# Kernel tuning notes

Measured on AMD Instinct MI355X. Metric: run time of the kernel, lower is better.

## Reference

```python
import jax, jax.numpy as jnp
import numpy as np


def reference(x, phi, sigma, M_phi_plus, M_phi_minus, M_u, padded_sl):
    """STU forward: spectral FFT convolution + autoregressive input term.

    x:   (B, L, D) input sequence
    phi: (L, K) time-domain spectral filters (top-K Hankel eigenvectors);
         V = rfft(phi, n=padded_sl) matches the module's precomputed V.
    sigma: (K,) Hankel eigenvalues
    M_phi_plus/minus: (K, D, D) per-filter projections
    M_u: (k_u, D, D) AR-on-input matrices
    """
    B, L, D = x.shape
    K = sigma.shape[0]
    n = padded_sl  # FFT length for causal linear convolution

    # Alternating-sign trick for the 'minus' featurization:
    # sum_j (-1)^j phi_j u_{t-j} = (-1)^t * conv(phi, sgn*u)_t
    sgn = jnp.where(jnp.arange(L) % 2 == 0, 1.0, -1.0).astype(x.dtype)[None, :, None]  # (1,L,1)

    V = jnp.fft.rfft(phi, n=n, axis=0)                       # (n//2+1, K) complex
    U = jnp.fft.rfft(jnp.stack([x, x * sgn], axis=-1), n=n, axis=1)  # (B, n//2+1, D, 2)
    prod = V[None, :, :, None, None] * U[:, :, None, :, :]    # (B, n//2+1, K, D, 2)
    conv = jnp.fft.irfft(prod, n=n, axis=1)[:, :L]            # (B, L, K, D, 2) causal conv
    U_plus = conv[..., 0]
    U_minus = conv[..., 1] * sgn[..., None]                   # undo sign on output side

    # Fold sigma^{1/4} scaling into the projection matrices.
    sig4 = (sigma ** 0.25).astype(x.dtype)[:, None, None]     # (K,1,1)
    spectral = (
        jnp.einsum('blkd,kdo->blo', U_plus, M_phi_plus * sig4)
        + jnp.einsum('blkd,kdo->blo', U_minus, M_phi_minus * sig4)
    )

    # compute_ar_u: y_t += sum_{i=0}^{k_u-1} x_{t-i} @ M_u[i]  (use_ar_u=True)
    ar_u = jnp.einsum('bld,do->blo', x, M_u[0])
    for i in range(1, M_u.shape[0]):  # small fixed depth k_u=3
        x_shift = jnp.pad(x, ((0, 0), (i, 0), (0, 0)))[:, :L]
        ar_u = ar_u + jnp.einsum('bld,do->blo', x_shift, M_u[i])

    # use_ar_y=False branch; dropout=0 (identity)
    return spectral + ar_u


def setup_inputs() -> dict:
    key = jax.random.key(0)
    ks = jax.random.split(key, 6)
    B, L, D, K, KU, N = 1, 2048, 768, 16, 3, 4096
    x = jax.random.normal(ks[0], (B, L, D), jnp.float32)
    phi = jax.random.normal(ks[1], (L, K), jnp.float32) / np.sqrt(L).astype(np.float32)
    sigma = jax.random.uniform(ks[2], (K,), jnp.float32, 0.1, 1.0)
    M_phi_plus = jax.random.normal(ks[3], (K, D, D), jnp.float32) * 0.02
    M_phi_minus = jax.random.normal(ks[4], (K, D, D), jnp.float32) * 0.02
    M_u = jax.random.normal(ks[5], (KU, D, D), jnp.float32) * 0.02
    return {"x": x, "phi": phi, "sigma": sigma, "M_phi_plus": M_phi_plus,
            "M_phi_minus": M_phi_minus, "M_u": M_u, "padded_sl": N}
```

## Files before the change

### kernel.cpp

```cpp
#include <hip/hip_runtime.h>

typedef __attribute__((ext_vector_type(8))) short bf16x8;
typedef __attribute__((ext_vector_type(8))) short short8;
typedef __attribute__((ext_vector_type(4))) float f32x4;

#define SL 2048
#define DM 768
#define NCH 32
#define MSPEC 24576
#define MTOT  26880

#define SPLITK 10
#define KSLICE 2688
#define NT2 42
#define NITER2 21

#define WS_U      0
#define WS_TMAT   110100480ULL
#define WS_XT     126910464ULL
#define WS_MCAT   130056192ULL
#define WS_PART   171343872ULL
#define WS_NEED   234258432ULL

#define NB_M   5040
#define NB_T   4104
#define NB_AR  768
#define NB_XT  384
#define NB_ALL (NB_M + NB_T + NB_AR + NB_XT)

__device__ __forceinline__ short f2bf(float f) {
  unsigned u = __builtin_bit_cast(unsigned, f);
  u = (u + 0x7FFFu + ((u >> 16) & 1u)) >> 16;
  return (short)u;
}

__device__ __forceinline__ void gload16(const short* g, short* l) {
  __builtin_amdgcn_global_load_lds(
      (const __attribute__((address_space(1))) void*)g,
      (__attribute__((address_space(3))) void*)l, 16, 0, 0);
}


__global__ __launch_bounds__(256) void k_zero(float4* out) {
  out[blockIdx.x * 256 + threadIdx.x] = float4{0.f, 0.f, 0.f, 0.f};
}

__global__ __launch_bounds__(256) void k_prep_all(const float* __restrict__ x,
                                                  const float* __restrict__ phi,
                                                  const float* __restrict__ sigma,
                                                  const float* __restrict__ Mp,
                                                  const float* __restrict__ Mm,
                                                  const float* __restrict__ Mu,
                                                  short* __restrict__ xT,
                                                  short* __restrict__ U,
                                                  short* __restrict__ Tmat,
                                                  short* __restrict__ McatT) {
  __shared__ short tile[64][65];
  const int b = blockIdx.x;
  const int t = threadIdx.x;

  if (b < NB_M) {
    const int m0 = (b % 420) * 64, o0 = (b / 420) * 64;
#pragma unroll
    for (int rr = 0; rr < 16; ++rr) {
      int ml = rr * 4 + (t >> 6), ol = t & 63;
      int m = m0 + ml, o = o0 + ol;
      float v;
      if (m < MSPEC) {
        int c = m / DM, d = m - c * DM;
        int k = c & 15;
        float s4 = sqrtf(sqrtf(sigma[k]));
        if (c < 16) v = Mp[((size_t)c * DM + d) * DM + o] * s4;
        else        v = Mm[((size_t)(c - 16) * DM + d) * DM + o] * s4;
      } else {
        int mm = m - MSPEC;
        int i = mm / DM, d = mm - i * DM;
        v = Mu[((size_t)i * DM + d) * DM + o];
      }
      tile[ml][ol] = f2bf(v);
    }
    __syncthreads();
#pragma unroll
    for (int rr = 0; rr < 16; ++rr) {
      int ol = rr * 4 + (t >> 6), ml = t & 63;
      McatT[(size_t)(o0 + ol) * MTOT + m0 + ml] = tile[ml][ol];
    }
    return;
  }
  if (b < NB_M + NB_T) {
    int idx = ((b - NB_M) * 256 + t) * 8;
    int c = idx >> 18;
    short8 v = {0, 0, 0, 0, 0, 0, 0, 0};
    if (c < 32) {
      int b0 = idx & 127, a = (idx >> 7) & 127, dlag = (idx >> 14) & 15;
      int j0 = dlag * 128 + a - b0;
#pragma unroll
      for (int e = 0; e < 8; ++e) {
        int j = j0 - e;
        if (j >= 0) {
          float p = phi[j * 16 + (c & 15)];
          if (c >= 16 && (j & 1)) p = -p;
          v[e] = f2bf(p);
        }
      }
    }
    *reinterpret_cast<short8*>(&Tmat[idx]) = v;
    return;
  }
  if (b < NB_M + NB_T + NB_AR) {
    int tid = (b - NB_M - NB_T) * 256 + t;
    int l = tid / 96, d0 = (tid - l * 96) * 8;
#pragma unroll
    for (int i = 0; i < 3; ++i) {
      short8 v = {0, 0, 0, 0, 0, 0, 0, 0};
      if (l >= i) {
        const float* src = &x[(size_t)(l - i) * DM + d0];
#pragma unroll
        for (int e = 0; e < 8; ++e) v[e] = f2bf(src[e]);
      }
      *reinterpret_cast<short8*>(&U[(size_t)l * MTOT + MSPEC + i * DM + d0]) = v;
    }
    return;
  }
  {
    const int bb = b - NB_M - NB_T - NB_AR;
    const int d0 = (bb % 12) * 64, l0 = (bb / 12) * 64;
#pragma unroll
    for (int rr = 0; rr < 16; ++rr) {
      int ll = rr * 4 + (t >> 6), dl = t & 63;
      tile[ll][dl] = f2bf(x[(size_t)(l0 + ll) * DM + d0 + dl]);
    }
    __syncthreads();
#pragma unroll
    for (int rr = 0; rr < 16; ++rr) {
      int dl = rr * 4 + (t >> 6), ll = t & 63;
      xT[(size_t)(d0 + dl) * SL + l0 + ll] = tile[ll][dl];
    }
  }
}


#define LDSREADS(BUF, KS, MQ)                                                   \
    _Pragma("unroll")                                                           \
    for (int q_ = 0; q_ < 4; ++q_)                                              \
      af_[q_] = *reinterpret_cast<const bf16x8*>(                               \
          &As[BUF][KS][wm1][((MQ) * 64 + q_ * 16 + lrow) * 32 + foff]);         \
    if ((MQ) == 0) {                                                            \
      _Pragma("unroll")                                                         \
      for (int i_ = 0; i_ < 4; ++i_)                                            \
        bf_[i_] = *reinterpret_cast<const bf16x8*>(                             \
            &Bs[BUF][KS][hB][(rB0 + i_ * 16 + lrow) * 32 + foff]);              \
    }

#define DOMFMA(MQ)                                                              \
    _Pragma("unroll")                                                           \
    for (int q_ = 0; q_ < 4; ++q_)                                              \
      _Pragma("unroll")                                                         \
      for (int i_ = 0; i_ < 4; ++i_)                                            \
        acc[(MQ) * 4 + q_][i_] = __builtin_amdgcn_mfma_f32_16x16x32_bf16(       \
            af_[q_], bf_[i_], acc[(MQ) * 4 + q_][i_], 0, 0, 0)

#define PHASE(BUF, KS, MQ, VMODE, STG) do {                                     \
    bf16x8 af_[4];                                                              \
    if ((VMODE) == 1) asm volatile("s_waitcnt vmcnt(6)" ::: "memory");          \
    if ((VMODE) == 2) {                                                         \
      if (j < nIterM1) asm volatile("s_waitcnt vmcnt(6)" ::: "memory");         \
      else             asm volatile("s_waitcnt vmcnt(0)" ::: "memory");         \
    }                                                                           \
    if ((VMODE) == 0) { LDSREADS(BUF, KS, MQ) }                                 \
    STG;                                                                        \
    if ((VMODE) != 0) {                                                         \
      __builtin_amdgcn_s_barrier();                                             \
      asm volatile("" ::: "memory");                                            \
      LDSREADS(BUF, KS, MQ)                                                     \
    }                                                                           \
    __builtin_amdgcn_s_setprio(1);                                              \
    DOMFMA(MQ);                                                                 \
    __builtin_amdgcn_s_setprio(0);                                              \
    asm volatile("s_waitcnt lgkmcnt(0)" ::: "memory");                          \
    __builtin_amdgcn_s_barrier();                                               \
  } while (0)


#define STA1(SBUF, SKS, SKT) do { int kt_ = (SKT); if (kt_ < nT) {              \
    int kch_ = kt_ * 64 + (SKS) * 32;                                           \
    int kb_ = kch_ >> 7, bo_ = kch_ & 127;                                      \
    int dl_ = 2 * rt - kb_;                                                     \
    const short* g0_ = (dl_ >= 0) ? (Tc + ((size_t)dl_ << 14) + bo_)            \
                                  : (Tz + bo_);                                 \
    const short* g1_ = Tc + ((size_t)(dl_ + 1) << 14) + bo_;                    \
    gload16(g0_, &As[SBUF][SKS][0][t8]);                                        \
    gload16(g1_, &As[SBUF][SKS][1][t8]); } } while (0)

#define STB1(SBUF, SKS, SKT) do { int kt_ = (SKT); if (kt_ < nT) {              \
    const short* g_ = Bb + kt_ * 64 + (SKS) * 32;                               \
    gload16(g_, &Bs[SBUF][SKS][0][t8]);                                         \
    gload16(g_ + (size_t)128 * SL, &Bs[SBUF][SKS][1][t8]); } } while (0)

__global__ __launch_bounds__(512, 2) void k_gemm1_8p(const short* __restrict__ Tmat,
                                                     const short* __restrict__ xT,
                                                     short* __restrict__ U) {
  __shared__ __align__(16) short As[2][2][2][4096];
  __shared__ __align__(16) short Bs[2][2][2][4096];
  const int bid = blockIdx.x;
  const int xcd = bid & 7;
  const int slot = bid >> 3;
  const int c = xcd * 4 + (slot & 3);
  const int q = slot >> 2;
  const int ct = q % 3;
  const int rt = 7 - q / 3;
  const int nT = 4 * (rt + 1);
  const int nIter = 2 * (rt + 1);
  const int nIterM1 = nIter - 1;
  const int t = threadIdx.x;
  const int lane = t & 63, wave = t >> 6;
  const int wm1 = wave >> 2;
  const int hB = (wave & 3) >> 1;
  const int rB0 = (wave & 1) * 64;
  const int lrow = lane & 15, quad = lane >> 4;
  const int foff = (quad ^ ((lrow >> 1) & 3)) << 3;
  const int r = t >> 2;
  const int cswz = ((t & 3) ^ ((r >> 1) & 3)) << 3;
  const int t8 = t * 8;

  const short* Tc = Tmat + ((size_t)(c * 16) << 14) + r * 128 + cswz;
  const short* Tz = Tmat + ((size_t)512 << 14) + r * 128 + cswz;
  const short* Bb = xT + (size_t)(ct * 256 + r) * SL + cswz;

  f32x4 acc[8][4] = {};

  STB1(0, 0, 0); STA1(0, 0, 0); STB1(0, 1, 0); STA1(0, 1, 0);
  STB1(1, 0, 1); STA1(1, 0, 1); STB1(1, 1, 1);

  for (int j = 0; j < nIter; ++j) {
    bf16x8 bf_[4];
    PHASE(0, 0, 0, 1, STA1(1, 1, 2 * j + 1));
    PHASE(0, 0, 1, 0, STB1(0, 0, 2 * j + 2));
    PHASE(0, 1, 0, 0, STA1(0, 0, 2 * j + 2));
    PHASE(0, 1, 1, 0, STB1(0, 1, 2 * j + 2));
    PHASE(1, 0, 0, 2, STA1(0, 1, 2 * j + 2));
    PHASE(1, 0, 1, 0, STB1(1, 0, 2 * j + 3));
    PHASE(1, 1, 0, 0, STA1(1, 0, 2 * j + 3));
    PHASE(1, 1, 1, 0, STB1(1, 1, 2 * j + 3));
  }

  const int wm128 = (wave >> 2) * 128, wn64 = (wave & 3) * 64;
  const int l0 = rt * 256, colbase = c * DM + ct * 256;
#pragma unroll
  for (int im = 0; im < 8; ++im)
#pragma unroll
    for (int in = 0; in < 4; ++in)
#pragma unroll
      for (int r4 = 0; r4 < 4; ++r4) {
        int row = l0 + wm128 + im * 16 + quad * 4 + r4;
        int col = colbase + wn64 + in * 16 + lrow;
        U[(size_t)row * MTOT + col] = f2bf(acc[im][in][r4]);
      }
}


#define STA2(SBUF, SKS, SKT) do { int kt_ = (SKT); if (kt_ < NT2) {             \
    const short* g_ = Abase + kt_ * 64 + (SKS) * 32;                            \
    gload16(g_, &As[SBUF][SKS][0][t8]);                                         \
    gload16(g_ + (size_t)128 * MTOT, &As[SBUF][SKS][1][t8]); } } while (0)

#define STB2(SBUF, SKS, SKT) do { int kt_ = (SKT); if (kt_ < NT2) {             \
    const short* g_ = Bbase + kt_ * 64 + (SKS) * 32;                            \
    gload16(g_, &Bs[SBUF][SKS][0][t8]);                                         \
    gload16(g_ + (size_t)128 * MTOT, &Bs[SBUF][SKS][1][t8]); } } while (0)

__global__ __launch_bounds__(512, 2) void k_gemm2_8p(const short* __restrict__ U,
                                                     const short* __restrict__ McatT,
                                                     float* __restrict__ out,
                                                     float* __restrict__ part,
                                                     int use_part) {
  __shared__ __align__(16) short As[2][2][2][4096];
  __shared__ __align__(16) short Bs[2][2][2][4096];
  const int bid = blockIdx.x;
  const int tile = bid % 24, kc = bid / 24;
  const int mt = tile & 7, nt_ = tile >> 3;
  const int m0 = mt * 256, o0 = nt_ * 256;
  const int kbase = kc * KSLICE;
  const int t = threadIdx.x;
  const int lane = t & 63, wave = t >> 6;
  const int wm1 = wave >> 2;
  const int hB = (wave & 3) >> 1;
  const int rB0 = (wave & 1) * 64;
  const int lrow = lane & 15, quad = lane >> 4;
  const int foff = (quad ^ ((lrow >> 1) & 3)) << 3;
  const int r = t >> 2;
  const int cswz = ((t & 3) ^ ((r >> 1) & 3)) << 3;
  const int t8 = t * 8;
  const int nIterM1 = NITER2 - 1;

  const short* Abase = U     + (size_t)(m0 + r) * MTOT + kbase + cswz;
  const short* Bbase = McatT + (size_t)(o0 + r) * MTOT + kbase + cswz;

  f32x4 acc[8][4] = {};

  STB2(0, 0, 0); STA2(0, 0, 0); STB2(0, 1, 0); STA2(0, 1, 0);
  STB2(1, 0, 1); STA2(1, 0, 1); STB2(1, 1, 1);

  for (int j = 0; j < NITER2; ++j) {
    bf16x8 bf_[4];
    PHASE(0, 0, 0, 1, STA2(1, 1, 2 * j + 1));
    PHASE(0, 0, 1, 0, STB2(0, 0, 2 * j + 2));
    PHASE(0, 1, 0, 0, STA2(0, 0, 2 * j + 2));
    PHASE(0, 1, 1, 0, STB2(0, 1, 2 * j + 2));
    PHASE(1, 0, 0, 2, STA2(0, 1, 2 * j + 2));
    PHASE(1, 0, 1, 0, STB2(1, 0, 2 * j + 3));
    PHASE(1, 1, 0, 0, STA2(1, 0, 2 * j + 3));
    PHASE(1, 1, 1, 0, STB2(1, 1, 2 * j + 3));
  }

  const int wm128 = (wave >> 2) * 128, wn64 = (wave & 3) * 64;
  if (use_part) {
    float* dst = part + (size_t)kc * (2048 * 768);
#pragma unroll
    for (int im = 0; im < 8; ++im)
#pragma unroll
      for (int in = 0; in < 4; ++in)
#pragma unroll
        for (int r4 = 0; r4 < 4; ++r4) {
          int row = m0 + wm128 + im * 16 + quad * 4 + r4;
          int col = o0 + wn64 + in * 16 + lrow;
          dst[(size_t)row * DM + col] = acc[im][in][r4];
        }
  } else {
#pragma unroll
    for (int im = 0; im < 8; ++im)
#pragma unroll
      for (int in = 0; in < 4; ++in)
#pragma unroll
        for (int r4 = 0; r4 < 4; ++r4) {
          int row = m0 + wm128 + im * 16 + quad * 4 + r4;
          int col = o0 + wn64 + in * 16 + lrow;
          atomicAdd(&out[(size_t)row * DM + col], acc[im][in][r4]);
        }
  }
}

__global__ __launch_bounds__(256) void k_reduce(const float4* __restrict__ part,
                                                float4* __restrict__ out) {
  int i = blockIdx.x * 256 + threadIdx.x;
  float4 s = part[i];
#pragma unroll
  for (int k = 1; k < SPLITK; ++k) {
    float4 v = part[(size_t)k * 393216 + i];
    s.x += v.x; s.y += v.y; s.z += v.z; s.w += v.w;
  }
  out[i] = s;
}

extern "C" void kernel_launch(void* const* d_in, const int* in_sizes, int n_in,
                              void* d_out, int out_size, void* d_ws, size_t ws_size,
                              hipStream_t stream) {
  (void)in_sizes; (void)n_in; (void)out_size;
  const float* x     = (const float*)d_in[0];
  const float* phi   = (const float*)d_in[1];
  const float* sigma = (const float*)d_in[2];
  const float* Mp    = (const float*)d_in[3];
  const float* Mm    = (const float*)d_in[4];
  const float* Mu    = (const float*)d_in[5];
  float* out = (float*)d_out;
  char* ws = (char*)d_ws;

  short* U     = (short*)(ws + WS_U);
  short* Tmat  = (short*)(ws + WS_TMAT);
  short* xT    = (short*)(ws + WS_XT);
  short* McatT = (short*)(ws + WS_MCAT);
  float* Wpart = (float*)(ws + WS_PART);
  const int use_part = ws_size >= WS_NEED ? 1 : 0;

  if (!use_part)
    k_zero<<<dim3(1536), dim3(256), 0, stream>>>((float4*)out);
  k_prep_all<<<dim3(NB_ALL), dim3(256), 0, stream>>>(x, phi, sigma, Mp, Mm, Mu,
                                                     xT, U, Tmat, McatT);
  k_gemm1_8p<<<dim3(768), dim3(512), 0, stream>>>(Tmat, xT, U);
  k_gemm2_8p<<<dim3(240), dim3(512), 0, stream>>>(U, McatT, out, Wpart, use_part);
  if (use_part)
    k_reduce<<<dim3(1536), dim3(256), 0, stream>>>((const float4*)Wpart, (float4*)out);
}
```

Baseline: 367.3 us.

## Transpose MFMA operands for vectorized epilogue stores and branchless clamped tile loads

Swaps the A/B operands of the MFMA so each lane holds four consecutive output columns. The GEMM epilogues can then write packed short4 bf16 and float4 partials instead of scalar strided stores. The Toeplitz matrix layout gains a leading zero block per channel (17 blocks instead of 16), so negative-lag loads read real zeros without a separate pointer. Out-of-range tile loads are clamped to the last tile instead of branched around, which removes divergent conditionals at the cost of redundant loads and a slightly larger workspace.

```diff
diff --git a/kernel.cpp b/kernel.cpp
--- a/kernel.cpp
+++ b/kernel.cpp
@@ -2,6 +2,7 @@
 
 typedef __attribute__((ext_vector_type(8))) short bf16x8;
 typedef __attribute__((ext_vector_type(8))) short short8;
+typedef __attribute__((ext_vector_type(4))) short short4v;
 typedef __attribute__((ext_vector_type(4))) float f32x4;
 
 #define SL 2048
@@ -15,15 +16,15 @@
 #define NT2 42
 #define NITER2 21
 
-#define WS_U      0
+#define WS_U      0ULL
 #define WS_TMAT   110100480ULL
-#define WS_XT     126910464ULL
-#define WS_MCAT   130056192ULL
-#define WS_PART   171343872ULL
-#define WS_NEED   234258432ULL
+#define WS_XT     127926272ULL
+#define WS_MCAT   131072000ULL
+#define WS_PART   172359680ULL
+#define WS_NEED   235274240ULL
 
 #define NB_M   5040
-#define NB_T   4104
+#define NB_T   4352
 #define NB_AR  768
 #define NB_XT  384
 #define NB_ALL (NB_M + NB_T + NB_AR + NB_XT)
@@ -89,10 +90,13 @@
   }
   if (b < NB_M + NB_T) {
     int idx = ((b - NB_M) * 256 + t) * 8;
-    int c = idx >> 18;
+    int blk = idx >> 14;
+    int c = blk / 17;
+    int w = blk - c * 17;
     short8 v = {0, 0, 0, 0, 0, 0, 0, 0};
-    if (c < 32) {
-      int b0 = idx & 127, a = (idx >> 7) & 127, dlag = (idx >> 14) & 15;
+    if (w > 0) {
+      int dlag = w - 1;
+      int b0 = idx & 127, a = (idx >> 7) & 127;
       int j0 = dlag * 128 + a - b0;
 #pragma unroll
       for (int e = 0; e < 8; ++e) {
@@ -158,7 +162,7 @@
       _Pragma("unroll")                                                         \
       for (int i_ = 0; i_ < 4; ++i_)                                            \
         acc[(MQ) * 4 + q_][i_] = __builtin_amdgcn_mfma_f32_16x16x32_bf16(       \
-            af_[q_], bf_[i_], acc[(MQ) * 4 + q_][i_], 0, 0, 0)
+            bf_[i_], af_[q_], acc[(MQ) * 4 + q_][i_], 0, 0, 0)
 
 #define PHASE(BUF, KS, MQ, VMODE, STG) do {                                     \
     bf16x8 af_[4];                                                              \
@@ -182,20 +186,19 @@
   } while (0)
 
 
-#define STA1(SBUF, SKS, SKT) do { int kt_ = (SKT); if (kt_ < nT) {              \
+#define STA1(SBUF, SKS, SKT) do {                                               \
+    int kt_ = (SKT); kt_ = kt_ < nTm1 ? kt_ : nTm1;                             \
     int kch_ = kt_ * 64 + (SKS) * 32;                                           \
     int kb_ = kch_ >> 7, bo_ = kch_ & 127;                                      \
-    int dl_ = 2 * rt - kb_;                                                     \
-    const short* g0_ = (dl_ >= 0) ? (Tc + ((size_t)dl_ << 14) + bo_)            \
-                                  : (Tz + bo_);                                 \
-    const short* g1_ = Tc + ((size_t)(dl_ + 1) << 14) + bo_;                    \
+    const short* g0_ = Tc + ((size_t)(2 * rt - kb_) << 14) + bo_;               \
     gload16(g0_, &As[SBUF][SKS][0][t8]);                                        \
-    gload16(g1_, &As[SBUF][SKS][1][t8]); } } while (0)
-
-#define STB1(SBUF, SKS, SKT) do { int kt_ = (SKT); if (kt_ < nT) {              \
+    gload16(g0_ + 16384, &As[SBUF][SKS][1][t8]); } while (0)
+
+#define STB1(SBUF, SKS, SKT) do {                                               \
+    int kt_ = (SKT); kt_ = kt_ < nTm1 ? kt_ : nTm1;                             \
     const short* g_ = Bb + kt_ * 64 + (SKS) * 32;                               \
     gload16(g_, &Bs[SBUF][SKS][0][t8]);                                         \
-    gload16(g_ + (size_t)128 * SL, &Bs[SBUF][SKS][1][t8]); } } while (0)
+    gload16(g_ + (size_t)128 * SL, &Bs[SBUF][SKS][1][t8]); } while (0)
 
 __global__ __launch_bounds__(512, 2) void k_gemm1_8p(const short* __restrict__ Tmat,
                                                      const short* __restrict__ xT,
@@ -210,6 +213,7 @@
   const int ct = q % 3;
   const int rt = 7 - q / 3;
   const int nT = 4 * (rt + 1);
+  const int nTm1 = nT - 1;
   const int nIter = 2 * (rt + 1);
   const int nIterM1 = nIter - 1;
   const int t = threadIdx.x;
@@ -223,8 +227,7 @@
   const int cswz = ((t & 3) ^ ((r >> 1) & 3)) << 3;
   const int t8 = t * 8;
 
-  const short* Tc = Tmat + ((size_t)(c * 16) << 14) + r * 128 + cswz;
-  const short* Tz = Tmat + ((size_t)512 << 14) + r * 128 + cswz;
+  const short* Tc = Tmat + ((size_t)(c * 17 + 1) << 14) + r * 128 + cswz;
   const short* Bb = xT + (size_t)(ct * 256 + r) * SL + cswz;
 
   f32x4 acc[8][4] = {};
@@ -247,27 +250,31 @@
   const int wm128 = (wave >> 2) * 128, wn64 = (wave & 3) * 64;
   const int l0 = rt * 256, colbase = c * DM + ct * 256;
 #pragma unroll
-  for (int im = 0; im < 8; ++im)
-#pragma unroll
-    for (int in = 0; in < 4; ++in)
-#pragma unroll
-      for (int r4 = 0; r4 < 4; ++r4) {
-        int row = l0 + wm128 + im * 16 + quad * 4 + r4;
-        int col = colbase + wn64 + in * 16 + lrow;
-        U[(size_t)row * MTOT + col] = f2bf(acc[im][in][r4]);
-      }
-}
-
-
-#define STA2(SBUF, SKS, SKT) do { int kt_ = (SKT); if (kt_ < NT2) {             \
+  for (int im = 0; im < 8; ++im) {
+    int row = l0 + wm128 + im * 16 + lrow;
+#pragma unroll
+    for (int in = 0; in < 4; ++in) {
+      int col = colbase + wn64 + in * 16 + quad * 4;
+      short4v v;
+#pragma unroll
+      for (int r4 = 0; r4 < 4; ++r4) v[r4] = f2bf(acc[im][in][r4]);
+      *reinterpret_cast<short4v*>(&U[(size_t)row * MTOT + col]) = v;
+    }
+  }
+}
+
+
+#define STA2(SBUF, SKS, SKT) do {                                               \
+    int kt_ = (SKT); kt_ = kt_ < NT2 - 1 ? kt_ : NT2 - 1;                       \
     const short* g_ = Abase + kt_ * 64 + (SKS) * 32;                            \
     gload16(g_, &As[SBUF][SKS][0][t8]);                                         \
-    gload16(g_ + (size_t)128 * MTOT, &As[SBUF][SKS][1][t8]); } } while (0)
-
-#define STB2(SBUF, SKS, SKT) do { int kt_ = (SKT); if (kt_ < NT2) {             \
+    gload16(g_ + (size_t)128 * MTOT, &As[SBUF][SKS][1][t8]); } while (0)
+
+#define STB2(SBUF, SKS, SKT) do {                                               \
+    int kt_ = (SKT); kt_ = kt_ < NT2 - 1 ? kt_ : NT2 - 1;                       \
     const short* g_ = Bbase + kt_ * 64 + (SKS) * 32;                            \
     gload16(g_, &Bs[SBUF][SKS][0][t8]);                                         \
-    gload16(g_ + (size_t)128 * MTOT, &Bs[SBUF][SKS][1][t8]); } } while (0)
+    gload16(g_ + (size_t)128 * MTOT, &Bs[SBUF][SKS][1][t8]); } while (0)
 
 __global__ __launch_bounds__(512, 2) void k_gemm2_8p(const short* __restrict__ U,
                                                      const short* __restrict__ McatT,
@@ -317,26 +324,27 @@
   if (use_part) {
     float* dst = part + (size_t)kc * (2048 * 768);
 #pragma unroll
-    for (int im = 0; im < 8; ++im)
-#pragma unroll
-      for (int in = 0; in < 4; ++in)
-#pragma unroll
-        for (int r4 = 0; r4 < 4; ++r4) {
-          int row = m0 + wm128 + im * 16 + quad * 4 + r4;
-          int col = o0 + wn64 + in * 16 + lrow;
-          dst[(size_t)row * DM + col] = acc[im][in][r4];
-        }
+    for (int im = 0; im < 8; ++im) {
+      int row = m0 + wm128 + im * 16 + lrow;
+#pragma unroll
+      for (int in = 0; in < 4; ++in) {
+        int col = o0 + wn64 + in * 16 + quad * 4;
+        float4 v = {acc[im][in][0], acc[im][in][1], acc[im][in][2], acc[im][in][3]};
+        *reinterpret_cast<float4*>(&dst[(size_t)row * DM + col]) = v;
+      }
+    }
   } else {
 #pragma unroll
-    for (int im = 0; im < 8; ++im)
-#pragma unroll
-      for (int in = 0; in < 4; ++in)
-#pragma unroll
-        for (int r4 = 0; r4 < 4; ++r4) {
-          int row = m0 + wm128 + im * 16 + quad * 4 + r4;
-          int col = o0 + wn64 + in * 16 + lrow;
-          atomicAdd(&out[(size_t)row * DM + col], acc[im][in][r4]);
-        }
+    for (int im = 0; im < 8; ++im) {
+      int row = m0 + wm128 + im * 16 + lrow;
+#pragma unroll
+      for (int in = 0; in < 4; ++in) {
+        int col = o0 + wn64 + in * 16 + quad * 4;
+#pragma unroll
+        for (int r4 = 0; r4 < 4; ++r4)
+          atomicAdd(&out[(size_t)row * DM + col + r4], acc[im][in][r4]);
+      }
+    }
   }
 }
 
```

Result: slower. 383.2 us (+4.3%).

## Replace 8-phase gemm2 pipeline with simple double-buffered loop and split-K 21

Applied to the files above, without the earlier changes.

The second GEMM drops its 8-phase, 4-stage software pipeline in favour of a plain double-buffered loop over 32-wide K steps, with a __syncthreads per step. Shared memory per block is halved and launch bounds now allow 4 blocks per CU. When the workspace is large enough, split-K goes from 10 to 21 (504 blocks) to fill the GPU better, at the cost of more partial-sum traffic in the reduce. The simpler pipeline gives up much of the latency hiding within a block and depends on higher occupancy to cover it instead.

```diff
diff --git a/kernel.cpp b/kernel.cpp
--- a/kernel.cpp
+++ b/kernel.cpp
@@ -10,17 +10,13 @@
 #define MSPEC 24576
 #define MTOT  26880
 
-#define SPLITK 10
-#define KSLICE 2688
-#define NT2 42
-#define NITER2 21
-
-#define WS_U      0
+#define WS_U      0ULL
 #define WS_TMAT   110100480ULL
 #define WS_XT     126910464ULL
 #define WS_MCAT   130056192ULL
 #define WS_PART   171343872ULL
-#define WS_NEED   234258432ULL
+#define WS_NEED10 234258432ULL
+#define WS_NEED21 303464448ULL
 
 #define NB_M   5040
 #define NB_T   4104
@@ -259,28 +255,18 @@
 }
 
 
-#define STA2(SBUF, SKS, SKT) do { int kt_ = (SKT); if (kt_ < NT2) {             \
-    const short* g_ = Abase + kt_ * 64 + (SKS) * 32;                            \
-    gload16(g_, &As[SBUF][SKS][0][t8]);                                         \
-    gload16(g_ + (size_t)128 * MTOT, &As[SBUF][SKS][1][t8]); } } while (0)
-
-#define STB2(SBUF, SKS, SKT) do { int kt_ = (SKT); if (kt_ < NT2) {             \
-    const short* g_ = Bbase + kt_ * 64 + (SKS) * 32;                            \
-    gload16(g_, &Bs[SBUF][SKS][0][t8]);                                         \
-    gload16(g_ + (size_t)128 * MTOT, &Bs[SBUF][SKS][1][t8]); } } while (0)
-
-__global__ __launch_bounds__(512, 2) void k_gemm2_8p(const short* __restrict__ U,
+template<int KSL, int NS>
+__global__ __launch_bounds__(512, 4) void k_gemm2_2p(const short* __restrict__ U,
                                                      const short* __restrict__ McatT,
                                                      float* __restrict__ out,
                                                      float* __restrict__ part,
                                                      int use_part) {
-  __shared__ __align__(16) short As[2][2][2][4096];
-  __shared__ __align__(16) short Bs[2][2][2][4096];
+  __shared__ __align__(16) short As[2][2][4096];
+  __shared__ __align__(16) short Bs[2][2][4096];
   const int bid = blockIdx.x;
   const int tile = bid % 24, kc = bid / 24;
   const int mt = tile & 7, nt_ = tile >> 3;
   const int m0 = mt * 256, o0 = nt_ * 256;
-  const int kbase = kc * KSLICE;
   const int t = threadIdx.x;
   const int lane = t & 63, wave = t >> 6;
   const int wm1 = wave >> 2;
@@ -291,31 +277,57 @@
   const int r = t >> 2;
   const int cswz = ((t & 3) ^ ((r >> 1) & 3)) << 3;
   const int t8 = t * 8;
-  const int nIterM1 = NITER2 - 1;
-
-  const short* Abase = U     + (size_t)(m0 + r) * MTOT + kbase + cswz;
-  const short* Bbase = McatT + (size_t)(o0 + r) * MTOT + kbase + cswz;
+
+  const short* Abase = U     + (size_t)(m0 + r) * MTOT + kc * KSL + cswz;
+  const short* Bbase = McatT + (size_t)(o0 + r) * MTOT + kc * KSL + cswz;
 
   f32x4 acc[8][4] = {};
 
-  STB2(0, 0, 0); STA2(0, 0, 0); STB2(0, 1, 0); STA2(0, 1, 0);
-  STB2(1, 0, 1); STA2(1, 0, 1); STB2(1, 1, 1);
-
-  for (int j = 0; j < NITER2; ++j) {
-    bf16x8 bf_[4];
-    PHASE(0, 0, 0, 1, STA2(1, 1, 2 * j + 1));
-    PHASE(0, 0, 1, 0, STB2(0, 0, 2 * j + 2));
-    PHASE(0, 1, 0, 0, STA2(0, 0, 2 * j + 2));
-    PHASE(0, 1, 1, 0, STB2(0, 1, 2 * j + 2));
-    PHASE(1, 0, 0, 2, STA2(0, 1, 2 * j + 2));
-    PHASE(1, 0, 1, 0, STB2(1, 0, 2 * j + 3));
-    PHASE(1, 1, 0, 0, STA2(1, 0, 2 * j + 3));
-    PHASE(1, 1, 1, 0, STB2(1, 1, 2 * j + 3));
+  auto stA = [&](int buf, int s) {
+    const short* g = Abase + s * 32;
+    gload16(g, &As[buf][0][t8]);
+    gload16(g + (size_t)128 * MTOT, &As[buf][1][t8]);
+  };
+  auto stB = [&](int buf, int s) {
+    const short* g = Bbase + s * 32;
+    gload16(g, &Bs[buf][0][t8]);
+    gload16(g + (size_t)128 * MTOT, &Bs[buf][1][t8]);
+  };
+
+  stA(0, 0); stB(0, 0);
+  int cur = 0;
+  for (int s = 0; s < NS; ++s) {
+    __syncthreads();
+    if (s + 1 < NS) { stA(cur ^ 1, s + 1); stB(cur ^ 1, s + 1); }
+    bf16x8 af0[4], af1[4], bf[4];
+#pragma unroll
+    for (int i = 0; i < 4; ++i)
+      bf[i] = *reinterpret_cast<const bf16x8*>(
+          &Bs[cur][hB][(rB0 + i * 16 + lrow) * 32 + foff]);
+#pragma unroll
+    for (int q = 0; q < 4; ++q)
+      af0[q] = *reinterpret_cast<const bf16x8*>(
+          &As[cur][wm1][(q * 16 + lrow) * 32 + foff]);
+#pragma unroll
+    for (int q = 0; q < 4; ++q)
+      af1[q] = *reinterpret_cast<const bf16x8*>(
+          &As[cur][wm1][(64 + q * 16 + lrow) * 32 + foff]);
+#pragma unroll
+    for (int q = 0; q < 4; ++q)
+#pragma unroll
+      for (int i = 0; i < 4; ++i)
+        acc[q][i] = __builtin_amdgcn_mfma_f32_16x16x32_bf16(af0[q], bf[i], acc[q][i], 0, 0, 0);
+#pragma unroll
+    for (int q = 0; q < 4; ++q)
+#pragma unroll
+      for (int i = 0; i < 4; ++i)
+        acc[4 + q][i] = __builtin_amdgcn_mfma_f32_16x16x32_bf16(af1[q], bf[i], acc[4 + q][i], 0, 0, 0);
+    cur ^= 1;
   }
 
   const int wm128 = (wave >> 2) * 128, wn64 = (wave & 3) * 64;
   if (use_part) {
-    float* dst = part + (size_t)kc * (2048 * 768);
+    float* dst = part + (size_t)kc * (SL * DM);
 #pragma unroll
     for (int im = 0; im < 8; ++im)
 #pragma unroll
@@ -341,11 +353,10 @@
 }
 
 __global__ __launch_bounds__(256) void k_reduce(const float4* __restrict__ part,
-                                                float4* __restrict__ out) {
+                                                float4* __restrict__ out, int nk) {
   int i = blockIdx.x * 256 + threadIdx.x;
   float4 s = part[i];
-#pragma unroll
-  for (int k = 1; k < SPLITK; ++k) {
+  for (int k = 1; k < nk; ++k) {
     float4 v = part[(size_t)k * 393216 + i];
     s.x += v.x; s.y += v.y; s.z += v.z; s.w += v.w;
   }
@@ -370,14 +381,21 @@
   short* xT    = (short*)(ws + WS_XT);
   short* McatT = (short*)(ws + WS_MCAT);
   float* Wpart = (float*)(ws + WS_PART);
-  const int use_part = ws_size >= WS_NEED ? 1 : 0;
-
-  if (!use_part)
+
+  const int mode = (ws_size >= WS_NEED21) ? 21 : (ws_size >= WS_NEED10 ? 10 : 0);
+
+  if (mode == 0)
     k_zero<<<dim3(1536), dim3(256), 0, stream>>>((float4*)out);
   k_prep_all<<<dim3(NB_ALL), dim3(256), 0, stream>>>(x, phi, sigma, Mp, Mm, Mu,
                                                      xT, U, Tmat, McatT);
   k_gemm1_8p<<<dim3(768), dim3(512), 0, stream>>>(Tmat, xT, U);
-  k_gemm2_8p<<<dim3(240), dim3(512), 0, stream>>>(U, McatT, out, Wpart, use_part);
-  if (use_part)
-    k_reduce<<<dim3(1536), dim3(256), 0, stream>>>((const float4*)Wpart, (float4*)out);
-}
+  if (mode == 21) {
+    k_gemm2_2p<1280, 40><<<dim3(504), dim3(512), 0, stream>>>(U, McatT, out, Wpart, 1);
+    k_reduce<<<dim3(1536), dim3(256), 0, stream>>>((const float4*)Wpart, (float4*)out, 21);
+  } else if (mode == 10) {
+    k_gemm2_2p<2688, 84><<<dim3(240), dim3(512), 0, stream>>>(U, McatT, out, Wpart, 1);
+    k_reduce<<<dim3(1536), dim3(256), 0, stream>>>((const float4*)Wpart, (float4*)out, 10);
+  } else {
+    k_gemm2_2p<2688, 84><<<dim3(240), dim3(512), 0, stream>>>(U, McatT, out, Wpart, 0);
+  }
+}
```

Result: slower. 753.2 us (+105.1%).

## Replace second GEMM with smaller-tile 128x128 split-K-8 kernel using simple double buffering

Applied to the files above, without the earlier changes.

Swaps the heavily pipelined 256x256-tile, split-K-10 second GEMM (240 blocks of 512 threads) for a 128x128-tile, split-K-8 kernel with 768 blocks of 256 threads. Each block double-buffers 32-wide K steps, with one barrier per step. The aim is more blocks to fill the CUs and fewer partial buffers to reduce. In exchange, each tile reuses data less, the loads and MFMAs overlap less finely, and more barriers are hit per unit of work.

```diff
diff --git a/kernel.cpp b/kernel.cpp
--- a/kernel.cpp
+++ b/kernel.cpp
@@ -10,12 +10,7 @@
 #define MSPEC 24576
 #define MTOT  26880
 
-#define SPLITK 10
-#define KSLICE 2688
-#define NT2 42
-#define NITER2 21
-
-#define WS_U      0
+#define WS_U      0ULL
 #define WS_TMAT   110100480ULL
 #define WS_XT     126910464ULL
 #define WS_MCAT   130056192ULL
@@ -259,93 +254,91 @@
 }
 
 
-#define STA2(SBUF, SKS, SKT) do { int kt_ = (SKT); if (kt_ < NT2) {             \
-    const short* g_ = Abase + kt_ * 64 + (SKS) * 32;                            \
-    gload16(g_, &As[SBUF][SKS][0][t8]);                                         \
-    gload16(g_ + (size_t)128 * MTOT, &As[SBUF][SKS][1][t8]); } } while (0)
-
-#define STB2(SBUF, SKS, SKT) do { int kt_ = (SKT); if (kt_ < NT2) {             \
-    const short* g_ = Bbase + kt_ * 64 + (SKS) * 32;                            \
-    gload16(g_, &Bs[SBUF][SKS][0][t8]);                                         \
-    gload16(g_ + (size_t)128 * MTOT, &Bs[SBUF][SKS][1][t8]); } } while (0)
-
-__global__ __launch_bounds__(512, 2) void k_gemm2_8p(const short* __restrict__ U,
-                                                     const short* __restrict__ McatT,
-                                                     float* __restrict__ out,
-                                                     float* __restrict__ part,
-                                                     int use_part) {
-  __shared__ __align__(16) short As[2][2][2][4096];
-  __shared__ __align__(16) short Bs[2][2][2][4096];
-  const int bid = blockIdx.x;
-  const int tile = bid % 24, kc = bid / 24;
-  const int mt = tile & 7, nt_ = tile >> 3;
-  const int m0 = mt * 256, o0 = nt_ * 256;
-  const int kbase = kc * KSLICE;
+__global__ __launch_bounds__(256) void k_g2(const short* __restrict__ U,
+                                            const short* __restrict__ McatT,
+                                            float* __restrict__ out,
+                                            float* __restrict__ part,
+                                            int use_part) {
+  __shared__ __align__(16) short As[2][128 * 32];
+  __shared__ __align__(16) short Bs[2][128 * 32];
+  const int wid = blockIdx.x;
+  const int kc = wid & 7;
+  const int slot = wid >> 3;
+  const int otile = slot % 6;
+  const int lb = slot / 6;
   const int t = threadIdx.x;
   const int lane = t & 63, wave = t >> 6;
-  const int wm1 = wave >> 2;
-  const int hB = (wave & 3) >> 1;
-  const int rB0 = (wave & 1) * 64;
+  const int wm = (wave >> 1) * 64, wn = (wave & 1) * 64;
   const int lrow = lane & 15, quad = lane >> 4;
-  const int foff = (quad ^ ((lrow >> 1) & 3)) << 3;
-  const int r = t >> 2;
-  const int cswz = ((t & 3) ^ ((r >> 1) & 3)) << 3;
-  const int t8 = t * 8;
-  const int nIterM1 = NITER2 - 1;
-
-  const short* Abase = U     + (size_t)(m0 + r) * MTOT + kbase + cswz;
-  const short* Bbase = McatT + (size_t)(o0 + r) * MTOT + kbase + cswz;
-
-  f32x4 acc[8][4] = {};
-
-  STB2(0, 0, 0); STA2(0, 0, 0); STB2(0, 1, 0); STA2(0, 1, 0);
-  STB2(1, 0, 1); STA2(1, 0, 1); STB2(1, 1, 1);
-
-  for (int j = 0; j < NITER2; ++j) {
-    bf16x8 bf_[4];
-    PHASE(0, 0, 0, 1, STA2(1, 1, 2 * j + 1));
-    PHASE(0, 0, 1, 0, STB2(0, 0, 2 * j + 2));
-    PHASE(0, 1, 0, 0, STA2(0, 0, 2 * j + 2));
-    PHASE(0, 1, 1, 0, STB2(0, 1, 2 * j + 2));
-    PHASE(1, 0, 0, 2, STA2(0, 1, 2 * j + 2));
-    PHASE(1, 0, 1, 0, STB2(1, 0, 2 * j + 3));
-    PHASE(1, 1, 0, 0, STA2(1, 0, 2 * j + 3));
-    PHASE(1, 1, 1, 0, STB2(1, 1, 2 * j + 3));
-  }
-
-  const int wm128 = (wave >> 2) * 128, wn64 = (wave & 3) * 64;
+  const int l4 = lane >> 2, lq = lane & 3;
+  const int r0 = wave * 32 + l4;
+  const int swz = (lq ^ ((l4 >> 1) & 3)) * 8;
+  const int foff = ((quad ^ ((lrow >> 1) & 3)) << 3);
+
+  f32x4 acc[4][4] = {};
+  const short* Ab = U + (size_t)lb * 128 * MTOT + kc * 3360 + (size_t)r0 * MTOT + swz;
+  const short* Bb = McatT + (size_t)otile * 128 * MTOT + kc * 3360 + (size_t)r0 * MTOT + swz;
+
+  auto stage = [&](int s, int buf) {
+    short* lA = &As[buf][wave * 1024 + lane * 8];
+    short* lB = &Bs[buf][wave * 1024 + lane * 8];
+    gload16(Ab + s * 32, lA);
+    gload16(Ab + s * 32 + (size_t)16 * MTOT, lA + 512);
+    gload16(Bb + s * 32, lB);
+    gload16(Bb + s * 32 + (size_t)16 * MTOT, lB + 512);
+  };
+
+  stage(0, 0);
+  int cur = 0;
+  for (int s = 0; s < 105; ++s) {
+    __syncthreads();
+    if (s + 1 < 105) stage(s + 1, cur ^ 1);
+    bf16x8 af[4], bfr[4];
+#pragma unroll
+    for (int im = 0; im < 4; ++im)
+      af[im] = *reinterpret_cast<const bf16x8*>(&As[cur][(wm + im * 16 + lrow) * 32 + foff]);
+#pragma unroll
+    for (int in = 0; in < 4; ++in)
+      bfr[in] = *reinterpret_cast<const bf16x8*>(&Bs[cur][(wn + in * 16 + lrow) * 32 + foff]);
+#pragma unroll
+    for (int im = 0; im < 4; ++im)
+#pragma unroll
+      for (int in = 0; in < 4; ++in)
+        acc[im][in] = __builtin_amdgcn_mfma_f32_16x16x32_bf16(af[im], bfr[in], acc[im][in], 0, 0, 0);
+    cur ^= 1;
+  }
+  const int l0 = lb * 128, o0 = otile * 128;
   if (use_part) {
-    float* dst = part + (size_t)kc * (2048 * 768);
-#pragma unroll
-    for (int im = 0; im < 8; ++im)
+    float* dst = part + (size_t)kc * ((size_t)SL * DM);
+#pragma unroll
+    for (int im = 0; im < 4; ++im)
 #pragma unroll
       for (int in = 0; in < 4; ++in)
 #pragma unroll
         for (int r4 = 0; r4 < 4; ++r4) {
-          int row = m0 + wm128 + im * 16 + quad * 4 + r4;
-          int col = o0 + wn64 + in * 16 + lrow;
-          dst[(size_t)row * DM + col] = acc[im][in][r4];
+          int row = wm + im * 16 + quad * 4 + r4;
+          int col = wn + in * 16 + lrow;
+          dst[(size_t)(l0 + row) * DM + o0 + col] = acc[im][in][r4];
         }
   } else {
 #pragma unroll
-    for (int im = 0; im < 8; ++im)
+    for (int im = 0; im < 4; ++im)
 #pragma unroll
       for (int in = 0; in < 4; ++in)
 #pragma unroll
         for (int r4 = 0; r4 < 4; ++r4) {
-          int row = m0 + wm128 + im * 16 + quad * 4 + r4;
-          int col = o0 + wn64 + in * 16 + lrow;
-          atomicAdd(&out[(size_t)row * DM + col], acc[im][in][r4]);
+          int row = wm + im * 16 + quad * 4 + r4;
+          int col = wn + in * 16 + lrow;
+          atomicAdd(&out[(size_t)(l0 + row) * DM + o0 + col], acc[im][in][r4]);
         }
   }
 }
 
 __global__ __launch_bounds__(256) void k_reduce(const float4* __restrict__ part,
-                                                float4* __restrict__ out) {
+                                                float4* __restrict__ out, int nk) {
   int i = blockIdx.x * 256 + threadIdx.x;
   float4 s = part[i];
-#pragma unroll
-  for (int k = 1; k < SPLITK; ++k) {
+  for (int k = 1; k < nk; ++k) {
     float4 v = part[(size_t)k * 393216 + i];
     s.x += v.x; s.y += v.y; s.z += v.z; s.w += v.w;
   }
@@ -377,7 +370,7 @@
   k_prep_all<<<dim3(NB_ALL), dim3(256), 0, stream>>>(x, phi, sigma, Mp, Mm, Mu,
                                                      xT, U, Tmat, McatT);
   k_gemm1_8p<<<dim3(768), dim3(512), 0, stream>>>(Tmat, xT, U);
-  k_gemm2_8p<<<dim3(240), dim3(512), 0, stream>>>(U, McatT, out, Wpart, use_part);
+  k_g2<<<dim3(768), dim3(256), 0, stream>>>(U, McatT, out, Wpart, use_part);
   if (use_part)
-    k_reduce<<<dim3(1536), dim3(256), 0, stream>>>((const float4*)Wpart, (float4*)out);
-}
+    k_reduce<<<dim3(1536), dim3(256), 0, stream>>>((const float4*)Wpart, (float4*)out, 8);
+}
```

Result: slower. 380.2 us (+3.5%).
